# Optimization experiments

Hardware: AMD Instinct MI355X
Metric: run time of the kernel (lower is better)

Reference implementation:

```python
import jax, jax.numpy as jnp
import numpy as np

GRID = 128  # interior volume side
THRESH = 0.05
MAX_IT = 500


def setup_inputs() -> dict:
    key = jax.random.key(0)
    # label volume: 0=background, 1=grey matter (solve domain), 2=source, 3=sink
    image = jax.random.randint(key, (GRID, GRID, GRID), 0, 4).astype(jnp.float32)
    return {"image": image, "source_label": 2, "sink_label": 3}


def reference(image, source_label, sink_label):
    # zero-pad by 1 voxel on all sides (as in the torch module)
    img = jnp.pad(image, 1)
    h, w, d = img.shape
    # over-relaxation parameter recomputed from min dim (module overwrites self.wopt)
    wopt = jnp.float32(2.0 / (1.0 + np.pi / min(h, w, d)))

    # boundary conditions: sink -> 1, source -> 0 (zeros already), elsewhere 0
    init = jnp.where(img == sink_label, 1.0, 0.0).astype(jnp.float32)

    # red/black checkerboard restricted to grey-matter (image==1) cells
    i = jnp.arange(h)[:, None, None]
    j = jnp.arange(w)[None, :, None]
    k = jnp.arange(d)[None, None, :]
    parity = (i + j + k) % 2
    gm = (img == 1)
    black = (jnp.logical_and(parity == 0, gm)).reshape(-1).astype(jnp.float32)
    red = (jnp.logical_and(parity == 1, gm)).reshape(-1).astype(jnp.float32)

    v0 = init.reshape(-1)
    # FAITHFUL to the original raveled-offset choice: +-1, +-h, +-h*w
    # (the torch code ravels with strides (w*d, d, 1) but gathers with h/h*w).
    # For cubic padded grids all masked (interior) cells keep these offsets in-bounds,
    # so jnp.roll's wraparound only touches positions the mask discards.
    offs = (1, h, h * w)

    def nbr_sum(v):  # v[i-1]+v[i+1]+v[i-h]+v[i+h]+v[i-h*w]+v[i+h*w]
        s = jnp.zeros_like(v)
        for o in offs:
            s = s + jnp.roll(v, -o) + jnp.roll(v, o)
        return s

    def sweep(v, mask):
        adj = wopt * mask * (nbr_sum(v) - 6.0 * v) / 6.0
        return v + adj, jnp.sum(jnp.abs(adj))

    def body(state):
        v, it, _ = state
        v, dv_b = sweep(v, black)  # black half-sweep (Gauss-Seidel: reads pre-sweep v)
        v, dv_r = sweep(v, red)    # red half-sweep reads black-updated v
        return v, it + 1, dv_b + dv_r

    def cond(state):
        _, it, dv = state
        # original: run once, then continue while delta_v >= thresh and iterations <= 500
        return jnp.logical_or(it == 0, jnp.logical_and(dv >= THRESH, it <= MAX_IT))

    v, iterations, delta_v = jax.lax.while_loop(
        cond, body, (v0, jnp.int32(0), jnp.float32(0.0))
    )

    laplace_sol = v.reshape(h, w, d)[1:-1, 1:-1, 1:-1]
    return laplace_sol, iterations, delta_v
```

## Files before the change

### kernel.cpp

```cpp
#include <hip/hip_runtime.h>
#include <hip/hip_cooperative_groups.h>

namespace cg = cooperative_groups;
typedef unsigned long long u64;

#define G    128
#define GG   (G * G)
#define P    130
#define P2   (P * P)
#define NPAD (P * P * P)
#define NG   (G * G * G)
#define NB   512
#define NT   256
#define TOT  (NB * NT)
#define CH   (NG / NB)
#define CT   (CH / NT)
#define CAPC (640 * 1024)
#define SAFEP (P2 + P + 1)
#define NLEAD 8
#define NCH   (NB / NLEAD)

__device__ inline float LDV(const float* p) {
    return __hip_atomic_load((float*)p, __ATOMIC_RELAXED, __HIP_MEMORY_SCOPE_AGENT);
}
__device__ inline void STV(float* p, float x) {
    __hip_atomic_store(p, x, __ATOMIC_RELAXED, __HIP_MEMORY_SCOPE_AGENT);
}
__device__ inline u64 LDF(const u64* p) {
    return __hip_atomic_load((u64*)p, __ATOMIC_RELAXED, __HIP_MEMORY_SCOPE_AGENT);
}

__device__ inline float bred(float x, int t, float* s4) {
    for (int o = 32; o; o >>= 1) x += __shfl_down(x, o, 64);
    __syncthreads();
    if ((t & 63) == 0) s4[t >> 6] = x;
    __syncthreads();
    return ((s4[0] + s4[1]) + s4[2]) + s4[3];
}

__device__ inline float gbar2(u64* __restrict__ leaf, u64* __restrict__ lead,
                              int phase, int b, int t, float part) {
    asm volatile("s_waitcnt vmcnt(0)" ::: "memory");
    __syncthreads();
    const int slot = phase & 1;
    if (t == 0) {
        u64 w = ((u64)(unsigned)phase << 32) | (u64)__float_as_uint(part);
        __hip_atomic_store(&leaf[slot * NB + b], w, __ATOMIC_RELAXED,
                           __HIP_MEMORY_SCOPE_AGENT);
    }
    float lsum = 0.0f;
    if (t < 64) {
        if (b < NLEAD) {
            const u64* lp = &leaf[slot * NB + b * NCH + t];
            u64 w;
            for (;;) {
                w = LDF(lp);
                if ((int)(w >> 32) >= phase) break;
                __builtin_amdgcn_s_sleep(1);
            }
            float x = __uint_as_float((unsigned)w);
            for (int o = 32; o; o >>= 1) x = __fadd_rn(x, __shfl_down(x, o, 64));
            if (t == 0) {
                u64 lw = ((u64)(unsigned)phase << 32) | (u64)__float_as_uint(x);
                __hip_atomic_store(&lead[slot * NLEAD + b], lw, __ATOMIC_RELAXED,
                                   __HIP_MEMORY_SCOPE_AGENT);
            }
        }
        const u64* gp = &lead[slot * NLEAD + (t & 7)];
        u64 w;
        for (;;) {
            w = LDF(gp);
            if (__all((int)(w >> 32) >= phase)) break;
            __builtin_amdgcn_s_sleep(1);
        }
        float pay = __uint_as_float((unsigned)w);
        lsum = __shfl(pay, 0, 64);
        lsum = __fadd_rn(lsum, __shfl(pay, 1, 64));
        lsum = __fadd_rn(lsum, __shfl(pay, 2, 64));
        lsum = __fadd_rn(lsum, __shfl(pay, 3, 64));
        lsum = __fadd_rn(lsum, __shfl(pay, 4, 64));
        lsum = __fadd_rn(lsum, __shfl(pay, 5, 64));
        lsum = __fadd_rn(lsum, __shfl(pay, 6, 64));
        lsum = __fadd_rn(lsum, __shfl(pay, 7, 64));
    }
    __syncthreads();
    return lsum;
}

__global__ __launch_bounds__(NT, 4)
void sor_kernel(const float* __restrict__ img, const int* __restrict__ sinkp,
                float* __restrict__ v, int* __restrict__ listB, int* __restrict__ listR,
                int* __restrict__ cntB, int* __restrict__ cntR,
                u64* __restrict__ leaf, u64* __restrict__ lead,
                float* __restrict__ out)
{
    cg::grid_group grid = cg::this_grid();
    const int t   = (int)threadIdx.x;
    const int b   = (int)blockIdx.x;
    const int tid = b * NT + t;
    const float wopt  = (float)(2.0 / (1.0 + 3.14159265358979323846 / 130.0));
    const float sinkf = (float)(*sinkp);

    __shared__ int   sB[NT], sR[NT];
    __shared__ float s4[4];
    __shared__ int   shN[4];

    if (t == 0) {
        __hip_atomic_store(&leaf[b],      0ull, __ATOMIC_RELAXED, __HIP_MEMORY_SCOPE_AGENT);
        __hip_atomic_store(&leaf[NB + b], 0ull, __ATOMIC_RELAXED, __HIP_MEMORY_SCOPE_AGENT);
        if (b < NLEAD) {
            __hip_atomic_store(&lead[b],         0ull, __ATOMIC_RELAXED, __HIP_MEMORY_SCOPE_AGENT);
            __hip_atomic_store(&lead[NLEAD + b], 0ull, __ATOMIC_RELAXED, __HIP_MEMORY_SCOPE_AGENT);
        }
    }

    for (int p = tid; p < NPAD; p += TOT) {
        int i = p / P2;
        int r = p - i * P2;
        int j = r / P;
        int k = r - j * P;
        float vv = 0.0f;
        if (i > 0 && i < P - 1 && j > 0 && j < P - 1 && k > 0 && k < P - 1) {
            float lab = img[(i - 1) * GG + (j - 1) * G + (k - 1)];
            vv = (lab == sinkf) ? 1.0f : 0.0f;
        }
        v[p] = vv;
    }

    const int g0 = b * CH + t * CT;
    int cB = 0, cR = 0;
    for (int q = 0; q < CT; ++q) {
        float lab = img[g0 + q];
        if (lab == 1.0f) {
            int g = g0 + q;
            int par = ((g >> 14) + ((g >> 7) & 127) + (g & 127)) & 1;
            if (par) cB++; else cR++;
        }
    }
    sB[t] = cB; sR[t] = cR;
    __syncthreads();
    for (int off = 1; off < NT; off <<= 1) {
        int aB = 0, aR = 0;
        if (t >= off) { aB = sB[t - off]; aR = sR[t - off]; }
        __syncthreads();
        if (t >= off) { sB[t] += aB; sR[t] += aR; }
        __syncthreads();
    }
    const int exB = sB[t] - cB;
    const int exR = sR[t] - cR;
    if (t == NT - 1) { cntB[b] = sB[t]; cntR[b] = sR[t]; }
    grid.sync();

    {
        int mB = 0, mR = 0, tB = 0, tR = 0;
        for (int e = t; e < NB; e += NT) {
            int vb = cntB[e], vr = cntR[e];
            tB += vb; tR += vr;
            if (e < b) { mB += vb; mR += vr; }
        }
        sB[t] = mB; sR[t] = mR;
        __syncthreads();
        for (int st = NT / 2; st > 0; st >>= 1) {
            if (t < st) { sB[t] += sB[t + st]; sR[t] += sR[t + st]; }
            __syncthreads();
        }
        if (t == 0) { shN[0] = sB[0]; shN[1] = sR[0]; }
        __syncthreads();
        sB[t] = tB; sR[t] = tR;
        __syncthreads();
        for (int st = NT / 2; st > 0; st >>= 1) {
            if (t < st) { sB[t] += sB[t + st]; sR[t] += sR[t + st]; }
            __syncthreads();
        }
        if (t == 0) { shN[2] = sB[0]; shN[3] = sR[0]; }
        __syncthreads();
    }
    const int baseB = shN[0], baseR = shN[1];
    const int nBt = shN[2], nRt = shN[3];

    {
        int pB = baseB + exB, pR = baseR + exR;
        for (int q = 0; q < CT; ++q) {
            int g = g0 + q;
            float lab = img[g];
            if (lab == 1.0f) {
                int i = g >> 14, j = (g >> 7) & 127, k = g & 127;
                int p = (i + 1) * P2 + (j + 1) * P + (k + 1);
                if ((i + j + k) & 1) listB[pB++] = p; else listR[pR++] = p;
            }
        }
    }
    grid.sync();

#define HOIST(LIST, NTOT, X, PV, NDV, SSV, D0, D1, D2, D3, D4, D5)          \
    {                                                                       \
        PV = -1; NDV = 0; SSV = 0.0f;                                       \
        D0 = SAFEP; D1 = SAFEP; D2 = SAFEP; D3 = SAFEP; D4 = SAFEP; D5 = SAFEP; \
        if ((X) < (NTOT)) {                                                 \
            const int p = LIST[X]; PV = p;                                  \
            const int pi = p / P2; const int rr = p - pi * P2;              \
            const int pj = rr / P; const int pk = rr - pj * P;              \
            const int i = pi - 1, j = pj - 1, k = pk - 1;                   \
            float ss = 0.0f; int nd = 0; int dd[6];                         \
            dd[0] = SAFEP; dd[1] = SAFEP; dd[2] = SAFEP;                    \
            dd[3] = SAFEP; dd[4] = SAFEP; dd[5] = SAFEP;                    \
            if (k + 1 <= G - 1) { float lb = img[i * GG + j * G + (k + 1)]; \
                if (lb == 1.0f) dd[nd++] = p + 1;                           \
                else ss = __fadd_rn(ss, (lb == sinkf) ? 1.0f : 0.0f); }     \
            if (k - 1 >= 0)     { float lb = img[i * GG + j * G + (k - 1)]; \
                if (lb == 1.0f) dd[nd++] = p - 1;                           \
                else ss = __fadd_rn(ss, (lb == sinkf) ? 1.0f : 0.0f); }     \
            if (j + 1 <= G - 1) { float lb = img[i * GG + (j + 1) * G + k]; \
                if (lb == 1.0f) dd[nd++] = p + P;                           \
                else ss = __fadd_rn(ss, (lb == sinkf) ? 1.0f : 0.0f); }     \
            if (j - 1 >= 0)     { float lb = img[i * GG + (j - 1) * G + k]; \
                if (lb == 1.0f) dd[nd++] = p - P;                           \
                else ss = __fadd_rn(ss, (lb == sinkf) ? 1.0f : 0.0f); }     \
            if (i + 1 <= G - 1) { float lb = img[(i + 1) * GG + j * G + k]; \
                if (lb == 1.0f) dd[nd++] = p + P2;                          \
                else ss = __fadd_rn(ss, (lb == sinkf) ? 1.0f : 0.0f); }     \
            if (i - 1 >= 0)     { float lb = img[(i - 1) * GG + j * G + k]; \
                if (lb == 1.0f) dd[nd++] = p - P2;                          \
                else ss = __fadd_rn(ss, (lb == sinkf) ? 1.0f : 0.0f); }     \
            NDV = nd; SSV = ss;                                             \
            D0 = dd[0]; D1 = dd[1]; D2 = dd[2];                             \
            D3 = dd[3]; D4 = dd[4]; D5 = dd[5];                             \
        }                                                                   \
    }

    int pB0, ndB0, dB00, dB01, dB02, dB03, dB04, dB05; float ssB0;
    int pB1, ndB1, dB10, dB11, dB12, dB13, dB14, dB15; float ssB1;
    int pR0, ndR0, dR00, dR01, dR02, dR03, dR04, dR05; float ssR0;
    int pR1, ndR1, dR10, dR11, dR12, dR13, dR14, dR15; float ssR1;
    HOIST(listB, nBt, tid,       pB0, ndB0, ssB0, dB00, dB01, dB02, dB03, dB04, dB05)
    HOIST(listB, nBt, tid + TOT, pB1, ndB1, ssB1, dB10, dB11, dB12, dB13, dB14, dB15)
    HOIST(listR, nRt, tid,       pR0, ndR0, ssR0, dR00, dR01, dR02, dR03, dR04, dR05)
    HOIST(listR, nRt, tid + TOT, pR1, ndR1, ssR1, dR10, dR11, dR12, dR13, dR14, dR15)

    float vB0 = 0.0f, vB1 = 0.0f, vR0 = 0.0f, vR1 = 0.0f;

#define CELL1(p, loc)                                                     \
    {                                                                     \
        float vc = LDV(&v[p]);                                            \
        float s = __fadd_rn(LDV(&v[(p) + 1]), LDV(&v[(p) - 1]));          \
        s = __fadd_rn(s, LDV(&v[(p) + P]));  s = __fadd_rn(s, LDV(&v[(p) - P]));   \
        s = __fadd_rn(s, LDV(&v[(p) + P2])); s = __fadd_rn(s, LDV(&v[(p) - P2]));  \
        float tt = __fsub_rn(s, __fmul_rn(6.0f, vc));                     \
        float adj = __fdiv_rn(__fmul_rn(wopt, tt), 6.0f);                 \
        STV(&v[p], __fadd_rn(vc, adj));                                   \
        loc = __fadd_rn(loc, fabsf(adj));                                 \
    }

#define SLOT_SWEEP2(ND0, SS0, V0, PP0, A0, A1, A2, A3, A4, A5,             \
                    ND1, SS1, V1, PP1, B0, B1, B2, B3, B4, B5, loc)        \
    {                                                                      \
        float x00 = (0 < ND0) ? LDV(&v[A0]) : 0.0f;                        \
        float x01 = (1 < ND0) ? LDV(&v[A1]) : 0.0f;                        \
        float x02 = (2 < ND0) ? LDV(&v[A2]) : 0.0f;                        \
        float x03 = (3 < ND0) ? LDV(&v[A3]) : 0.0f;                        \
        float x04 = (4 < ND0) ? LDV(&v[A4]) : 0.0f;                        \
        float x05 = (5 < ND0) ? LDV(&v[A5]) : 0.0f;                        \
        float x10 = (0 < ND1) ? LDV(&v[B0]) : 0.0f;                        \
        float x11 = (1 < ND1) ? LDV(&v[B1]) : 0.0f;                        \
        float x12 = (2 < ND1) ? LDV(&v[B2]) : 0.0f;                        \
        float x13 = (3 < ND1) ? LDV(&v[B3]) : 0.0f;                        \
        float x14 = (4 < ND1) ? LDV(&v[B4]) : 0.0f;                        \
        float x15 = (5 < ND1) ? LDV(&v[B5]) : 0.0f;                        \
        float s0 = __fadd_rn(x00, x01);                                    \
        s0 = __fadd_rn(s0, x02); s0 = __fadd_rn(s0, x03);                  \
        s0 = __fadd_rn(s0, x04); s0 = __fadd_rn(s0, x05);                  \
        s0 = __fadd_rn(s0, SS0);                                           \
        float s1 = __fadd_rn(x10, x11);                                    \
        s1 = __fadd_rn(s1, x12); s1 = __fadd_rn(s1, x13);                  \
        s1 = __fadd_rn(s1, x14); s1 = __fadd_rn(s1, x15);                  \
        s1 = __fadd_rn(s1, SS1);                                           \
        float t0 = __fsub_rn(s0, __fmul_rn(6.0f, V0));                     \
        float t1 = __fsub_rn(s1, __fmul_rn(6.0f, V1));                     \
        float adj0 = __fdiv_rn(__fmul_rn(wopt, t0), 6.0f);                 \
        float adj1 = __fdiv_rn(__fmul_rn(wopt, t1), 6.0f);                 \
        V0 = __fadd_rn(V0, adj0);                                          \
        V1 = __fadd_rn(V1, adj1);                                          \
        if (ND0 > 0) STV(&v[PP0], V0);                                     \
        if (ND1 > 0) STV(&v[PP1], V1);                                     \
        loc = __fadd_rn(loc, fabsf(adj0));                                 \
        loc = __fadd_rn(loc, fabsf(adj1));                                 \
    }

    int it = 0;
    float dv = 0.0f;
    int phase = 0;
    do {
        float locb = 0.0f;
        SLOT_SWEEP2(ndB0, ssB0, vB0, pB0, dB00, dB01, dB02, dB03, dB04, dB05,
                    ndB1, ssB1, vB1, pB1, dB10, dB11, dB12, dB13, dB14, dB15, locb)
        for (int x = tid + 2 * TOT; x < nBt; x += TOT) {
            const int p = listB[x];
            CELL1(p, locb)
        }
        float bs = bred(locb, t, s4);
        ++phase;
        float bacc = gbar2(leaf, lead, phase, b, t, bs);

        float locr = 0.0f;
        SLOT_SWEEP2(ndR0, ssR0, vR0, pR0, dR00, dR01, dR02, dR03, dR04, dR05,
                    ndR1, ssR1, vR1, pR1, dR10, dR11, dR12, dR13, dR14, dR15, locr)
        for (int x = tid + 2 * TOT; x < nRt; x += TOT) {
            const int p = listR[x];
            CELL1(p, locr)
        }
        float rs = bred(locr, t, s4);
        ++phase;
        float racc = gbar2(leaf, lead, phase, b, t, rs);

        if (t == 0) s4[0] = __fadd_rn(bacc, racc);
        __syncthreads();
        dv = s4[0];

        ++it;
    } while (dv >= 0.05f && it <= 500);

    if (pB0 >= 0 && ndB0 == 0) STV(&v[pB0], vB0);
    if (pB1 >= 0 && ndB1 == 0) STV(&v[pB1], vB1);
    if (pR0 >= 0 && ndR0 == 0) STV(&v[pR0], vR0);
    if (pR1 >= 0 && ndR1 == 0) STV(&v[pR1], vR1);
    ++phase;
    gbar2(leaf, lead, phase, b, t, 0.0f);

    for (int g = tid; g < NG; g += TOT) {
        int i = g >> 14, j = (g >> 7) & 127, k = g & 127;
        out[g] = LDV(&v[(i + 1) * P2 + (j + 1) * P + (k + 1)]);
    }
    if (tid == 0) {
        out[NG]     = (float)it;
        out[NG + 1] = dv;
    }
}

extern "C" void kernel_launch(void* const* d_in, const int* in_sizes, int n_in,
                              void* d_out, int out_size, void* d_ws, size_t ws_size,
                              hipStream_t stream) {
    const float* img  = (const float*)d_in[0];
    const int*   sink = (const int*)d_in[2];
    float*       out  = (float*)d_out;

    char* ws = (char*)d_ws;
    size_t off = 0;
    float* v = (float*)(ws + off);
    off += (size_t)NPAD * sizeof(float);
    off = (off + 255) & ~(size_t)255;
    int* listB = (int*)(ws + off);
    off += (size_t)CAPC * sizeof(int);
    int* listR = (int*)(ws + off);
    off += (size_t)CAPC * sizeof(int);
    int* cntB = (int*)(ws + off);
    off += (size_t)NB * sizeof(int);
    int* cntR = (int*)(ws + off);
    off += (size_t)NB * sizeof(int);
    off = (off + 255) & ~(size_t)255;
    u64* leaf = (u64*)(ws + off);
    off += (size_t)2 * NB * sizeof(u64);
    off = (off + 255) & ~(size_t)255;
    u64* lead = (u64*)(ws + off);
    off += (size_t)2 * NLEAD * sizeof(u64);
    (void)ws_size; (void)in_sizes; (void)n_in; (void)out_size;

    void* args[] = { (void*)&img, (void*)&sink, (void*)&v,
                     (void*)&listB, (void*)&listR, (void*)&cntB, (void*)&cntR,
                     (void*)&leaf, (void*)&lead, (void*)&out };
    hipLaunchCooperativeKernel((const void*)sor_kernel, dim3(NB), dim3(NT),
                               args, 0, stream);
}
```

Baseline: 5.390 ms.

## Keep block-local SOR values in shared-memory slabs with per-block cell lists

Each block now owns one contiguous 4096-cell slab, which is 32 j-rows of a single i-plane. The block keeps the current values of its grey-matter cells in shared memory. In-slab k and j neighbours are read from LDS, and only cross-block neighbours (i±1, and j at slab edges) go through global atomics. Cells store to global only when they have such outside neighbours. The global prefix-scan grid.sync is replaced by per-block lists capped at 768 entries per colour, held as three fixed slots per thread. This removes most global stencil traffic and the overflow loop. The trade-off is a hard per-block capacity that silently drops cells if a slab has more than 768 grey-matter cells of one parity.

```diff
diff --git a/kernel.cpp b/kernel.cpp
--- a/kernel.cpp
+++ b/kernel.cpp
@@ -14,9 +14,7 @@
 #define NT   256
 #define TOT  (NB * NT)
 #define CH   (NG / NB)
-#define CT   (CH / NT)
-#define CAPC (640 * 1024)
-#define SAFEP (P2 + P + 1)
+#define SEG  768
 #define NLEAD 8
 #define NCH   (NB / NLEAD)
 
@@ -90,7 +88,6 @@
 __global__ __launch_bounds__(NT, 4)
 void sor_kernel(const float* __restrict__ img, const int* __restrict__ sinkp,
                 float* __restrict__ v, int* __restrict__ listB, int* __restrict__ listR,
-                int* __restrict__ cntB, int* __restrict__ cntR,
                 u64* __restrict__ leaf, u64* __restrict__ lead,
                 float* __restrict__ out)
 {
@@ -101,9 +98,10 @@
     const float wopt  = (float)(2.0 / (1.0 + 3.14159265358979323846 / 130.0));
     const float sinkf = (float)(*sinkp);
 
+    __shared__ float slab[CH];
     __shared__ int   sB[NT], sR[NT];
     __shared__ float s4[4];
-    __shared__ int   shN[4];
+    __shared__ int   shN[2];
 
     if (t == 0) {
         __hip_atomic_store(&leaf[b],      0ull, __ATOMIC_RELAXED, __HIP_MEMORY_SCOPE_AGENT);
@@ -127,9 +125,11 @@
         v[p] = vv;
     }
 
-    const int g0 = b * CH + t * CT;
+    for (int x = t; x < CH; x += NT) slab[x] = 0.0f;
+
+    const int g0 = b * CH + t * (CH / NT);
     int cB = 0, cR = 0;
-    for (int q = 0; q < CT; ++q) {
+    for (int q = 0; q < CH / NT; ++q) {
         float lab = img[g0 + q];
         if (lab == 1.0f) {
             int g = g0 + q;
@@ -148,142 +148,98 @@
     }
     const int exB = sB[t] - cB;
     const int exR = sR[t] - cR;
-    if (t == NT - 1) { cntB[b] = sB[t]; cntR[b] = sR[t]; }
-    grid.sync();
+    if (t == NT - 1) { shN[0] = sB[t]; shN[1] = sR[t]; }
+    __syncthreads();
+    const int cntB = shN[0], cntR = shN[1];
 
     {
-        int mB = 0, mR = 0, tB = 0, tR = 0;
-        for (int e = t; e < NB; e += NT) {
-            int vb = cntB[e], vr = cntR[e];
-            tB += vb; tR += vr;
-            if (e < b) { mB += vb; mR += vr; }
-        }
-        sB[t] = mB; sR[t] = mR;
-        __syncthreads();
-        for (int st = NT / 2; st > 0; st >>= 1) {
-            if (t < st) { sB[t] += sB[t + st]; sR[t] += sR[t + st]; }
-            __syncthreads();
-        }
-        if (t == 0) { shN[0] = sB[0]; shN[1] = sR[0]; }
-        __syncthreads();
-        sB[t] = tB; sR[t] = tR;
-        __syncthreads();
-        for (int st = NT / 2; st > 0; st >>= 1) {
-            if (t < st) { sB[t] += sB[t + st]; sR[t] += sR[t + st]; }
-            __syncthreads();
-        }
-        if (t == 0) { shN[2] = sB[0]; shN[3] = sR[0]; }
-        __syncthreads();
-    }
-    const int baseB = shN[0], baseR = shN[1];
-    const int nBt = shN[2], nRt = shN[3];
-
-    {
-        int pB = baseB + exB, pR = baseR + exR;
-        for (int q = 0; q < CT; ++q) {
+        int pB = exB, pR = exR;
+        for (int q = 0; q < CH / NT; ++q) {
             int g = g0 + q;
             float lab = img[g];
             if (lab == 1.0f) {
+                int l = t * (CH / NT) + q;
                 int i = g >> 14, j = (g >> 7) & 127, k = g & 127;
-                int p = (i + 1) * P2 + (j + 1) * P + (k + 1);
-                if ((i + j + k) & 1) listB[pB++] = p; else listR[pR++] = p;
+                if ((i + j + k) & 1) { if (pB < SEG) listB[b * SEG + pB] = l; pB++; }
+                else                 { if (pR < SEG) listR[b * SEG + pR] = l; pR++; }
             }
         }
     }
+    __syncthreads();
+
     grid.sync();
 
-#define HOIST(LIST, NTOT, X, PV, NDV, SSV, D0, D1, D2, D3, D4, D5)          \
+#define HOIST(LIST, CNT, X, PV, LV, MV, SV)                                 \
     {                                                                       \
-        PV = -1; NDV = 0; SSV = 0.0f;                                       \
-        D0 = SAFEP; D1 = SAFEP; D2 = SAFEP; D3 = SAFEP; D4 = SAFEP; D5 = SAFEP; \
-        if ((X) < (NTOT)) {                                                 \
-            const int p = LIST[X]; PV = p;                                  \
-            const int pi = p / P2; const int rr = p - pi * P2;              \
-            const int pj = rr / P; const int pk = rr - pj * P;              \
-            const int i = pi - 1, j = pj - 1, k = pk - 1;                   \
-            float ss = 0.0f; int nd = 0; int dd[6];                         \
-            dd[0] = SAFEP; dd[1] = SAFEP; dd[2] = SAFEP;                    \
-            dd[3] = SAFEP; dd[4] = SAFEP; dd[5] = SAFEP;                    \
-            if (k + 1 <= G - 1) { float lb = img[i * GG + j * G + (k + 1)]; \
-                if (lb == 1.0f) dd[nd++] = p + 1;                           \
-                else ss = __fadd_rn(ss, (lb == sinkf) ? 1.0f : 0.0f); }     \
-            if (k - 1 >= 0)     { float lb = img[i * GG + j * G + (k - 1)]; \
-                if (lb == 1.0f) dd[nd++] = p - 1;                           \
-                else ss = __fadd_rn(ss, (lb == sinkf) ? 1.0f : 0.0f); }     \
-            if (j + 1 <= G - 1) { float lb = img[i * GG + (j + 1) * G + k]; \
-                if (lb == 1.0f) dd[nd++] = p + P;                           \
-                else ss = __fadd_rn(ss, (lb == sinkf) ? 1.0f : 0.0f); }     \
-            if (j - 1 >= 0)     { float lb = img[i * GG + (j - 1) * G + k]; \
-                if (lb == 1.0f) dd[nd++] = p - P;                           \
-                else ss = __fadd_rn(ss, (lb == sinkf) ? 1.0f : 0.0f); }     \
-            if (i + 1 <= G - 1) { float lb = img[(i + 1) * GG + j * G + k]; \
-                if (lb == 1.0f) dd[nd++] = p + P2;                          \
-                else ss = __fadd_rn(ss, (lb == sinkf) ? 1.0f : 0.0f); }     \
-            if (i - 1 >= 0)     { float lb = img[(i - 1) * GG + j * G + k]; \
-                if (lb == 1.0f) dd[nd++] = p - P2;                          \
-                else ss = __fadd_rn(ss, (lb == sinkf) ? 1.0f : 0.0f); }     \
-            NDV = nd; SSV = ss;                                             \
-            D0 = dd[0]; D1 = dd[1]; D2 = dd[2];                             \
-            D3 = dd[3]; D4 = dd[4]; D5 = dd[5];                             \
+        PV = -1; LV = 0; MV = 0; SV = 0.0f;                                 \
+        if ((X) < (CNT)) {                                                  \
+            const int l = LIST[b * SEG + (X)]; LV = l;                      \
+            const int g = b * CH + l;                                       \
+            const int i = g >> 14, j = (g >> 7) & 127, k = g & 127;         \
+            PV = (i + 1) * P2 + (j + 1) * P + (k + 1);                      \
+            int m = 0; float ss = 0.0f; float lb;                           \
+            if (k < 127) { lb = img[g + 1];                                 \
+                if (lb == 1.0f) m |= 1;                                     \
+                else ss = __fadd_rn(ss, (lb == sinkf) ? 1.0f : 0.0f); }     \
+            if (k > 0)   { lb = img[g - 1];                                 \
+                if (lb == 1.0f) m |= 2;                                     \
+                else ss = __fadd_rn(ss, (lb == sinkf) ? 1.0f : 0.0f); }     \
+            if (j < 127) { lb = img[g + G];                                 \
+                if (lb == 1.0f) m |= ((j & 31) != 31) ? 4 : 16;             \
+                else ss = __fadd_rn(ss, (lb == sinkf) ? 1.0f : 0.0f); }     \
+            if (j > 0)   { lb = img[g - G];                                 \
+                if (lb == 1.0f) m |= ((j & 31) != 0) ? 8 : 32;              \
+                else ss = __fadd_rn(ss, (lb == sinkf) ? 1.0f : 0.0f); }     \
+            if (i < 127) { lb = img[g + GG];                                \
+                if (lb == 1.0f) m |= 64;                                    \
+                else ss = __fadd_rn(ss, (lb == sinkf) ? 1.0f : 0.0f); }     \
+            if (i > 0)   { lb = img[g - GG];                                \
+                if (lb == 1.0f) m |= 128;                                   \
+                else ss = __fadd_rn(ss, (lb == sinkf) ? 1.0f : 0.0f); }     \
+            MV = m; SV = ss;                                                \
         }                                                                   \
     }
 
-    int pB0, ndB0, dB00, dB01, dB02, dB03, dB04, dB05; float ssB0;
-    int pB1, ndB1, dB10, dB11, dB12, dB13, dB14, dB15; float ssB1;
-    int pR0, ndR0, dR00, dR01, dR02, dR03, dR04, dR05; float ssR0;
-    int pR1, ndR1, dR10, dR11, dR12, dR13, dR14, dR15; float ssR1;
-    HOIST(listB, nBt, tid,       pB0, ndB0, ssB0, dB00, dB01, dB02, dB03, dB04, dB05)
-    HOIST(listB, nBt, tid + TOT, pB1, ndB1, ssB1, dB10, dB11, dB12, dB13, dB14, dB15)
-    HOIST(listR, nRt, tid,       pR0, ndR0, ssR0, dR00, dR01, dR02, dR03, dR04, dR05)
-    HOIST(listR, nRt, tid + TOT, pR1, ndR1, ssR1, dR10, dR11, dR12, dR13, dR14, dR15)
-
-    float vB0 = 0.0f, vB1 = 0.0f, vR0 = 0.0f, vR1 = 0.0f;
-
-#define CELL1(p, loc)                                                     \
-    {                                                                     \
-        float vc = LDV(&v[p]);                                            \
-        float s = __fadd_rn(LDV(&v[(p) + 1]), LDV(&v[(p) - 1]));          \
-        s = __fadd_rn(s, LDV(&v[(p) + P]));  s = __fadd_rn(s, LDV(&v[(p) - P]));   \
-        s = __fadd_rn(s, LDV(&v[(p) + P2])); s = __fadd_rn(s, LDV(&v[(p) - P2]));  \
-        float tt = __fsub_rn(s, __fmul_rn(6.0f, vc));                     \
-        float adj = __fdiv_rn(__fmul_rn(wopt, tt), 6.0f);                 \
-        STV(&v[p], __fadd_rn(vc, adj));                                   \
-        loc = __fadd_rn(loc, fabsf(adj));                                 \
-    }
-
-#define SLOT_SWEEP2(ND0, SS0, V0, PP0, A0, A1, A2, A3, A4, A5,             \
-                    ND1, SS1, V1, PP1, B0, B1, B2, B3, B4, B5, loc)        \
-    {                                                                      \
-        float x00 = (0 < ND0) ? LDV(&v[A0]) : 0.0f;                        \
-        float x01 = (1 < ND0) ? LDV(&v[A1]) : 0.0f;                        \
-        float x02 = (2 < ND0) ? LDV(&v[A2]) : 0.0f;                        \
-        float x03 = (3 < ND0) ? LDV(&v[A3]) : 0.0f;                        \
-        float x04 = (4 < ND0) ? LDV(&v[A4]) : 0.0f;                        \
-        float x05 = (5 < ND0) ? LDV(&v[A5]) : 0.0f;                        \
-        float x10 = (0 < ND1) ? LDV(&v[B0]) : 0.0f;                        \
-        float x11 = (1 < ND1) ? LDV(&v[B1]) : 0.0f;                        \
-        float x12 = (2 < ND1) ? LDV(&v[B2]) : 0.0f;                        \
-        float x13 = (3 < ND1) ? LDV(&v[B3]) : 0.0f;                        \
-        float x14 = (4 < ND1) ? LDV(&v[B4]) : 0.0f;                        \
-        float x15 = (5 < ND1) ? LDV(&v[B5]) : 0.0f;                        \
-        float s0 = __fadd_rn(x00, x01);                                    \
-        s0 = __fadd_rn(s0, x02); s0 = __fadd_rn(s0, x03);                  \
-        s0 = __fadd_rn(s0, x04); s0 = __fadd_rn(s0, x05);                  \
-        s0 = __fadd_rn(s0, SS0);                                           \
-        float s1 = __fadd_rn(x10, x11);                                    \
-        s1 = __fadd_rn(s1, x12); s1 = __fadd_rn(s1, x13);                  \
-        s1 = __fadd_rn(s1, x14); s1 = __fadd_rn(s1, x15);                  \
-        s1 = __fadd_rn(s1, SS1);                                           \
-        float t0 = __fsub_rn(s0, __fmul_rn(6.0f, V0));                     \
-        float t1 = __fsub_rn(s1, __fmul_rn(6.0f, V1));                     \
-        float adj0 = __fdiv_rn(__fmul_rn(wopt, t0), 6.0f);                 \
-        float adj1 = __fdiv_rn(__fmul_rn(wopt, t1), 6.0f);                 \
-        V0 = __fadd_rn(V0, adj0);                                          \
-        V1 = __fadd_rn(V1, adj1);                                          \
-        if (ND0 > 0) STV(&v[PP0], V0);                                     \
-        if (ND1 > 0) STV(&v[PP1], V1);                                     \
-        loc = __fadd_rn(loc, fabsf(adj0));                                 \
-        loc = __fadd_rn(loc, fabsf(adj1));                                 \
+    int pB0, lB0, mB0; float sB0;
+    int pB1, lB1, mB1; float sB1;
+    int pB2, lB2, mB2; float sB2;
+    int pR0, lR0, mR0; float sR0;
+    int pR1, lR1, mR1; float sR1;
+    int pR2, lR2, mR2; float sR2;
+    HOIST(listB, cntB, t,          pB0, lB0, mB0, sB0)
+    HOIST(listB, cntB, t + NT,     pB1, lB1, mB1, sB1)
+    HOIST(listB, cntB, t + 2 * NT, pB2, lB2, mB2, sB2)
+    HOIST(listR, cntR, t,          pR0, lR0, mR0, sR0)
+    HOIST(listR, cntR, t + NT,     pR1, lR1, mR1, sR1)
+    HOIST(listR, cntR, t + 2 * NT, pR2, lR2, mR2, sR2)
+
+    float vB0 = 0.0f, vB1 = 0.0f, vB2 = 0.0f;
+    float vR0 = 0.0f, vR1 = 0.0f, vR2 = 0.0f;
+
+#define CELLS(PV, LV, MV, SV, V, loc)                                       \
+    {                                                                       \
+        float xk1 = slab[(LV + 1) & (CH - 1)];                              \
+        float xk0 = slab[(LV - 1) & (CH - 1)];                              \
+        float xj1 = slab[(LV + G) & (CH - 1)];                              \
+        float xj0 = slab[(LV - G) & (CH - 1)];                              \
+        float a0 = (MV & 1) ? xk1 : 0.0f;                                   \
+        float a1 = (MV & 2) ? xk0 : 0.0f;                                   \
+        float a2 = (MV & 4) ? xj1 : ((MV & 16) ? LDV(&v[PV + P]) : 0.0f);   \
+        float a3 = (MV & 8) ? xj0 : ((MV & 32) ? LDV(&v[PV - P]) : 0.0f);   \
+        float a4 = (MV & 64)  ? LDV(&v[PV + P2]) : 0.0f;                    \
+        float a5 = (MV & 128) ? LDV(&v[PV - P2]) : 0.0f;                    \
+        float s = __fadd_rn(a0, a1);                                        \
+        s = __fadd_rn(s, a2); s = __fadd_rn(s, a3);                         \
+        s = __fadd_rn(s, a4); s = __fadd_rn(s, a5);                         \
+        s = __fadd_rn(s, SV);                                               \
+        float tt = __fsub_rn(s, __fmul_rn(6.0f, V));                        \
+        float adj = __fdiv_rn(__fmul_rn(wopt, tt), 6.0f);                   \
+        V = __fadd_rn(V, adj);                                              \
+        if (PV >= 0) {                                                      \
+            slab[LV] = V;                                                   \
+            if (MV & 0xF0) STV(&v[PV], V);                                  \
+        }                                                                   \
+        loc = __fadd_rn(loc, fabsf(adj));                                   \
     }
 
     int it = 0;
@@ -291,23 +247,17 @@
     int phase = 0;
     do {
         float locb = 0.0f;
-        SLOT_SWEEP2(ndB0, ssB0, vB0, pB0, dB00, dB01, dB02, dB03, dB04, dB05,
-                    ndB1, ssB1, vB1, pB1, dB10, dB11, dB12, dB13, dB14, dB15, locb)
-        for (int x = tid + 2 * TOT; x < nBt; x += TOT) {
-            const int p = listB[x];
-            CELL1(p, locb)
-        }
+        CELLS(pB0, lB0, mB0, sB0, vB0, locb)
+        CELLS(pB1, lB1, mB1, sB1, vB1, locb)
+        CELLS(pB2, lB2, mB2, sB2, vB2, locb)
         float bs = bred(locb, t, s4);
         ++phase;
         float bacc = gbar2(leaf, lead, phase, b, t, bs);
 
         float locr = 0.0f;
-        SLOT_SWEEP2(ndR0, ssR0, vR0, pR0, dR00, dR01, dR02, dR03, dR04, dR05,
-                    ndR1, ssR1, vR1, pR1, dR10, dR11, dR12, dR13, dR14, dR15, locr)
-        for (int x = tid + 2 * TOT; x < nRt; x += TOT) {
-            const int p = listR[x];
-            CELL1(p, locr)
-        }
+        CELLS(pR0, lR0, mR0, sR0, vR0, locr)
+        CELLS(pR1, lR1, mR1, sR1, vR1, locr)
+        CELLS(pR2, lR2, mR2, sR2, vR2, locr)
         float rs = bred(locr, t, s4);
         ++phase;
         float racc = gbar2(leaf, lead, phase, b, t, rs);
@@ -319,10 +269,12 @@
         ++it;
     } while (dv >= 0.05f && it <= 500);
 
-    if (pB0 >= 0 && ndB0 == 0) STV(&v[pB0], vB0);
-    if (pB1 >= 0 && ndB1 == 0) STV(&v[pB1], vB1);
-    if (pR0 >= 0 && ndR0 == 0) STV(&v[pR0], vR0);
-    if (pR1 >= 0 && ndR1 == 0) STV(&v[pR1], vR1);
+    if (pB0 >= 0 && !(mB0 & 0xF0)) STV(&v[pB0], vB0);
+    if (pB1 >= 0 && !(mB1 & 0xF0)) STV(&v[pB1], vB1);
+    if (pB2 >= 0 && !(mB2 & 0xF0)) STV(&v[pB2], vB2);
+    if (pR0 >= 0 && !(mR0 & 0xF0)) STV(&v[pR0], vR0);
+    if (pR1 >= 0 && !(mR1 & 0xF0)) STV(&v[pR1], vR1);
+    if (pR2 >= 0 && !(mR2 & 0xF0)) STV(&v[pR2], vR2);
     ++phase;
     gbar2(leaf, lead, phase, b, t, 0.0f);
 
@@ -349,13 +301,9 @@
     off += (size_t)NPAD * sizeof(float);
     off = (off + 255) & ~(size_t)255;
     int* listB = (int*)(ws + off);
-    off += (size_t)CAPC * sizeof(int);
+    off += (size_t)NB * SEG * sizeof(int);
     int* listR = (int*)(ws + off);
-    off += (size_t)CAPC * sizeof(int);
-    int* cntB = (int*)(ws + off);
-    off += (size_t)NB * sizeof(int);
-    int* cntR = (int*)(ws + off);
-    off += (size_t)NB * sizeof(int);
+    off += (size_t)NB * SEG * sizeof(int);
     off = (off + 255) & ~(size_t)255;
     u64* leaf = (u64*)(ws + off);
     off += (size_t)2 * NB * sizeof(u64);
@@ -365,7 +313,7 @@
     (void)ws_size; (void)in_sizes; (void)n_in; (void)out_size;
 
     void* args[] = { (void*)&img, (void*)&sink, (void*)&v,
-                     (void*)&listB, (void*)&listR, (void*)&cntB, (void*)&cntR,
+                     (void*)&listB, (void*)&listR,
                      (void*)&leaf, (void*)&lead, (void*)&out };
     hipLaunchCooperativeKernel((const void*)sor_kernel, dim3(NB), dim3(NT),
                                args, 0, stream);
```

New measurement: 6.313 ms. 1.17x slower.
